# Performance work log

Hardware: AMD Instinct MI355X
Metric: run time of the kernel (lower is better)

Reference implementation:

```python
import jax, jax.numpy as jnp
import numpy as np

K = 128           # top-k
NUM_SAMPLES = 500 # perturbation samples
SIGMA = 0.05      # noise scale (forward arg sigma in the torch module)


def setup_inputs() -> dict:
    key = jax.random.key(0)
    k1, k2 = jax.random.split(key)
    x = jax.random.normal(k1, (32, 2048), dtype=jnp.float32)
    noise = jax.random.normal(k2, (32, NUM_SAMPLES, 2048), dtype=jnp.float32)
    return {"x": x, "noise": noise}


def reference(x, noise):
    # x: (b, d) scores; noise: (b, n, d) standard-normal perturbations.
    b, d = x.shape
    n = noise.shape[1]
    perturbed = x[:, None, :] + noise * SIGMA          # (b, n, d)
    _, idx = jax.lax.top_k(perturbed, K)               # (b, n, K) indices into d
    idx = jnp.sort(idx, axis=-1)                       # sorted, matching torch.sort
    # indicators[b,j,d] = mean_n one_hot(idx[b,n,j], d)
    # Computed with a scatter-add instead of materializing the (b,n,K,d) one-hot.
    bi = jnp.arange(b)[:, None, None]                  # (b,1,1)
    ki = jnp.arange(K)[None, None, :]                  # (1,1,K)
    counts = jnp.zeros((b, K, d), dtype=x.dtype).at[bi, ki, idx].add(1.0)
    indicators = counts / n                            # (b, K, d)
    return indicators, idx
```

## Files before the change

### kernel.cpp

```cpp
#include <hip/hip_runtime.h>


constexpr int B_     = 32;
constexpr int D_     = 2048;
constexpr int NS_    = 500;
constexpr int TOPK_  = 128;
constexpr int SLACK_ = 32;
constexpr float SIGMA_  = 0.05f;
constexpr int PER_LANE_ = D_ / 64;
constexpr int HALF_  = D_ / 2;
constexpr int HPL_   = HALF_ / 64;
constexpr int CAP_   = 256;
constexpr int JCHUNK_ = 8;
constexpr int CUTBIT_END_ = 14;

__device__ __forceinline__ uint32_t order_key(float f) {
  uint32_t u = __float_as_uint(f);
  return (u & 0x80000000u) ? ~u : (u | 0x80000000u);
}
__device__ __forceinline__ float inv_key(uint32_t k) {
  uint32_t u = (k & 0x80000000u) ? (k & 0x7FFFFFFFu) : ~k;
  return __uint_as_float(u);
}

__global__ __launch_bounds__(64) void ptk_cutoff(const float* __restrict__ x,
                                                 float* __restrict__ cutf,
                                                 int* __restrict__ fb_cnt) {
  if (blockIdx.x == 0 && threadIdx.x == 0) fb_cnt[0] = 0;
  const int lane = threadIdx.x & 63;
  const int b = blockIdx.x;
  const float* __restrict__ xr = x + (size_t)b * D_;
  uint32_t keys[PER_LANE_];
#pragma unroll
  for (int j = 0; j < PER_LANE_; j += 4) {
    const float4 xv = *reinterpret_cast<const float4*>(xr + lane * PER_LANE_ + j);
    keys[j + 0] = order_key(xv.x); keys[j + 1] = order_key(xv.y);
    keys[j + 2] = order_key(xv.z); keys[j + 3] = order_key(xv.w);
  }
  uint32_t prefix = 0; int k = TOPK_ + SLACK_;
#pragma unroll 1
  for (int bit = 31; bit >= CUTBIT_END_; --bit) {
    const uint32_t want = (prefix >> bit) | 1u;
    int c = 0;
#pragma unroll
    for (int j = 0; j < PER_LANE_; ++j) c += ((keys[j] >> bit) == want) ? 1 : 0;
#pragma unroll
    for (int off = 32; off >= 1; off >>= 1) c += __shfl_xor(c, off);
    if (c >= k) prefix |= (1u << bit); else k -= c;
  }
  if (lane == 0) cutf[b] = inv_key(prefix);
}

template <int NSLOT>
__device__ __forceinline__ void finish_row(const uint2* __restrict__ comp,
                                           const int C0, const int C,
                                           float* __restrict__ idx_row,
                                           const int lane, const uint64_t below) {
  uint32_t kk[NSLOT], ki[NSLOT];
#pragma unroll
  for (int s = 0; s < NSLOT; ++s) {
    const int q = (s << 6) + lane;
    const int a = (q < C0) ? q : (CAP_ + q - C0);
    const uint2 v = (q < C) ? comp[a] : make_uint2(0u, 0u);
    kk[s] = v.x; ki[s] = v.y;
  }

  uint32_t orv = 0u, andv = 0xFFFFFFFFu;
#pragma unroll
  for (int s = 0; s < NSLOT; ++s) {
    const bool valid = ((s << 6) + lane) < C;
    orv  |= valid ? kk[s] : 0u;
    andv &= valid ? kk[s] : 0xFFFFFFFFu;
  }
#pragma unroll
  for (int off = 32; off >= 1; off >>= 1) {
    orv  |= __shfl_xor(orv, off);
    andv &= __shfl_xor(andv, off);
  }
  const uint32_t diff = orv ^ andv;

  uint32_t prefix; int r;
  if (diff == 0u) {
    prefix = orv; r = TOPK_;
  } else {
    const int startbit = 31 - __clz(diff);
    prefix = (startbit == 31) ? 0u : (andv & (0xFFFFFFFFu << (startbit + 1)));
    int k = TOPK_;
    int A = C;
#pragma unroll 1
    for (int bit = startbit; bit >= 0; --bit) {
      const uint32_t want = (prefix >> bit) | 1u;
      int c = 0;
#pragma unroll
      for (int s = 0; s < NSLOT; ++s)
        c += __popcll(__ballot((kk[s] >> bit) == want));
      if (c >= k) { prefix |= (1u << bit); A = c; }
      else        { k -= c; A -= c; }
      if (A == 1) {
        uint32_t mykey = 0u; bool have = false;
#pragma unroll
        for (int s = 0; s < NSLOT; ++s) {
          const bool valid = ((s << 6) + lane) < C;
          const bool hit = valid && ((kk[s] >> bit) == (prefix >> bit));
          mykey = hit ? kk[s] : mykey;
          have |= hit;
        }
        const uint64_t mb = __ballot(have);
        const int src = __ffsll((unsigned long long)mb) - 1;
        prefix = __shfl(mykey, src);
        k = 1;
        break;
      }
    }
    r = k;
  }

  int sel_run = 0, eq_run = 0;
#pragma unroll
  for (int s = 0; s < NSLOT; ++s) {
    const bool gt = kk[s] > prefix;
    const bool eq = kk[s] == prefix;
    const uint64_t meq = __ballot(eq);
    const int eqrank = eq_run + __popcll(meq & below);
    const bool sel = gt || (eq && (eqrank < r));
    const uint64_t msel = __ballot(sel);
    if (sel) {
      const int pos = sel_run + __popcll(msel & below);
      idx_row[pos] = (float)(int)ki[s];
    }
    sel_run += __popcll(msel);
    eq_run  += __popcll(meq);
  }
}

__global__ __launch_bounds__(256, 8) void ptk_select(
    const float* __restrict__ x, const float* __restrict__ noise,
    const float* __restrict__ cutf, float* __restrict__ out_idx,
    int* __restrict__ fb_cnt, int* __restrict__ fb_list) {
  __shared__ uint2 comp[2][2 * CAP_];
  __shared__ int cnts[2][2];

  const int lane = threadIdx.x & 63;
  const int wave = threadIdx.x >> 6;
  const int pair = wave >> 1;
  const int half = wave & 1;
  const int row  = blockIdx.x * 2 + pair;
  const int b = row / NS_;

  const float* __restrict__ xr = x + (size_t)b * D_ + half * HALF_;
  const float* __restrict__ nr = noise + (size_t)row * D_ + half * HALF_;
  const int base_l = lane * HPL_;
  const int base_i = half * HALF_ + base_l;

  float p[HPL_];
#pragma unroll
  for (int j = 0; j < HPL_; j += 4) {
    const float4 nv = *reinterpret_cast<const float4*>(nr + base_l + j);
    const float4 xv = *reinterpret_cast<const float4*>(xr + base_l + j);
    p[j + 0] = fmaf(SIGMA_, nv.x, xv.x);
    p[j + 1] = fmaf(SIGMA_, nv.y, xv.y);
    p[j + 2] = fmaf(SIGMA_, nv.z, xv.z);
    p[j + 3] = fmaf(SIGMA_, nv.w, xv.w);
  }

  const float cf = cutf[b];

  uint32_t m = 0;
#pragma unroll
  for (int j = 0; j < HPL_; ++j) m |= (p[j] >= cf) ? (1u << j) : 0u;
  const int cnt = __popc(m);

  const uint64_t below = (lane == 0) ? 0ull : ((~0ull) >> (64 - lane));
  int offset = 0, Cw = 0;
#pragma unroll
  for (int t = 0; t < 5; ++t) {
    const uint64_t mb = __ballot((cnt >> t) & 1);
    offset += (int)__popcll(mb & below) << t;
    Cw     += (int)__popcll(mb) << t;
  }
  if (lane == 0) cnts[pair][half] = Cw;

  {
    int q = half * CAP_ + offset;
#pragma unroll
    for (int j = 0; j < HPL_; ++j) {
      if (m & (1u << j)) {
        comp[pair][q] = make_uint2(order_key(p[j]), (uint32_t)(base_i + j));
        ++q;
      }
    }
  }
  __syncthreads();

  if (half) return;

  const int C0 = cnts[pair][0];
  const int C1 = cnts[pair][1];
  const int C  = C0 + C1;

  float* __restrict__ idx_row = out_idx + (size_t)row * TOPK_;

  if (C >= TOPK_ && C <= CAP_) {
    const uint2* cp = comp[pair];
    if (C <= 128)       finish_row<2>(cp, C0, C, idx_row, lane, below);
    else if (C <= 192)  finish_row<3>(cp, C0, C, idx_row, lane, below);
    else                finish_row<4>(cp, C0, C, idx_row, lane, below);
  } else {
    if (lane == 0) {
      const int p_ = atomicAdd(fb_cnt, 1);
      fb_list[p_] = row;
    }
  }
}

__global__ __launch_bounds__(64) void ptk_fb(
    const float* __restrict__ x, const float* __restrict__ noise,
    const int* __restrict__ fb_cnt, const int* __restrict__ fb_list,
    float* __restrict__ out_idx) {
  const int lane = threadIdx.x & 63;
  const int cnt = fb_cnt[0];
  for (int i = blockIdx.x; i < cnt; i += (int)gridDim.x) {
    const int row = fb_list[i];
    const int b = row / NS_;
    const float* __restrict__ xr = x + (size_t)b * D_;
    const float* __restrict__ nr = noise + (size_t)row * D_;
    float* __restrict__ idx_row = out_idx + (size_t)row * TOPK_;

    const int bi = lane * PER_LANE_;
    uint32_t keys[PER_LANE_];
#pragma unroll
    for (int j = 0; j < PER_LANE_; ++j)
      keys[j] = order_key(fmaf(SIGMA_, nr[bi + j], xr[bi + j]));

    uint32_t prefix = 0; int k = TOPK_;
#pragma unroll 1
    for (int bit = 31; bit >= 0; --bit) {
      const uint32_t want = (prefix >> bit) | 1u;
      int c = 0;
#pragma unroll
      for (int j = 0; j < PER_LANE_; ++j) c += ((keys[j] >> bit) == want) ? 1 : 0;
#pragma unroll
      for (int off = 32; off >= 1; off >>= 1) c += __shfl_xor(c, off);
      if (c >= k) prefix |= (1u << bit); else k -= c;
    }
    const int r = k;

    int gt = 0, eq = 0;
#pragma unroll
    for (int j = 0; j < PER_LANE_; ++j) {
      gt += (keys[j] > prefix) ? 1 : 0;
      eq += (keys[j] == prefix) ? 1 : 0;
    }
    uint32_t incl2 = (uint32_t)gt | ((uint32_t)eq << 16);
#pragma unroll
    for (int off = 1; off < 64; off <<= 1) {
      uint32_t y = __shfl_up(incl2, (unsigned)off);
      if (lane >= off) incl2 += y;
    }
    const int gt_base = (int)(incl2 & 0xFFFFu) - gt;
    const int eq_base = (int)(incl2 >> 16) - eq;
    int pos = gt_base + min(eq_base, r);
    int eq_seen = eq_base;
#pragma unroll
    for (int j = 0; j < PER_LANE_; ++j) {
      const uint32_t kj = keys[j];
      bool s = false;
      if (kj > prefix) s = true;
      else if (kj == prefix) { s = (eq_seen < r); eq_seen++; }
      if (s) { idx_row[pos] = (float)(bi + j); pos++; }
    }
  }
}

__global__ __launch_bounds__(256) void ptk_hist(
    const float* __restrict__ out_idx, float* __restrict__ indicators) {
  __shared__ int hist[JCHUNK_][D_];

  const int tid   = threadIdx.x;
  const int b     = blockIdx.x >> 4;
  const int chunk = blockIdx.x & 15;
  const int j0    = chunk * JCHUNK_;

  int4* h4 = (int4*)hist;
  for (int t = tid; t < JCHUNK_ * D_ / 4; t += 256)
    h4[t] = make_int4(0, 0, 0, 0);
  __syncthreads();

  const float* __restrict__ src = out_idx + (size_t)b * NS_ * TOPK_ + j0;
  for (int t = tid; t < NS_ * 2; t += 256) {
    const int n = t >> 1;
    const int q = (t & 1) << 2;
    const float4 v = *reinterpret_cast<const float4*>(src + (size_t)n * TOPK_ + q);
    atomicAdd(&hist[q + 0][(int)v.x], 1);
    atomicAdd(&hist[q + 1][(int)v.y], 1);
    atomicAdd(&hist[q + 2][(int)v.z], 1);
    atomicAdd(&hist[q + 3][(int)v.w], 1);
  }
  __syncthreads();

  float4* __restrict__ dst =
      (float4*)(indicators + ((size_t)b * TOPK_ + j0) * D_);
  for (int t = tid; t < JCHUNK_ * D_ / 4; t += 256) {
    const int4 h = h4[t];
    float4 o;
    o.x = (float)h.x / (float)NS_;
    o.y = (float)h.y / (float)NS_;
    o.z = (float)h.z / (float)NS_;
    o.w = (float)h.w / (float)NS_;
    dst[t] = o;
  }
}

extern "C" void kernel_launch(void* const* d_in, const int* in_sizes, int n_in,
                              void* d_out, int out_size, void* d_ws, size_t ws_size,
                              hipStream_t stream) {
  const float* x     = (const float*)d_in[0];
  const float* noise = (const float*)d_in[1];
  float* indicators  = (float*)d_out;
  float* out_idx     = (float*)d_out + (size_t)B_ * TOPK_ * D_;
  float* cutf        = (float*)d_ws;
  int*   fb_cnt      = (int*)d_ws + 64;
  int*   fb_list     = (int*)d_ws + 128;

  hipLaunchKernelGGL(ptk_cutoff, dim3(B_), dim3(64), 0, stream, x, cutf, fb_cnt);

  const int rows = B_ * NS_;
  hipLaunchKernelGGL(ptk_select, dim3(rows / 2), dim3(256), 0, stream,
                     x, noise, cutf, out_idx, fb_cnt, fb_list);

  hipLaunchKernelGGL(ptk_fb, dim3(64), dim3(64), 0, stream,
                     x, noise, fb_cnt, fb_list, out_idx);

  hipLaunchKernelGGL(ptk_hist, dim3(B_ * 16), dim3(256), 0, stream,
                     out_idx, indicators);
}
```

Baseline: 224.3 us.

## Fold fallback exact top-k into select kernel and drop separate fallback launch

After: 220.5 us. Within noise of the previous version (-1.7%).

```diff
diff --git a/kernel.cpp b/kernel.cpp
--- a/kernel.cpp
+++ b/kernel.cpp
@@ -24,9 +24,7 @@
 }
 
 __global__ __launch_bounds__(64) void ptk_cutoff(const float* __restrict__ x,
-                                                 float* __restrict__ cutf,
-                                                 int* __restrict__ fb_cnt) {
-  if (blockIdx.x == 0 && threadIdx.x == 0) fb_cnt[0] = 0;
+                                                 float* __restrict__ cutf) {
   const int lane = threadIdx.x & 63;
   const int b = blockIdx.x;
   const float* __restrict__ xr = x + (size_t)b * D_;
@@ -135,9 +133,8 @@
 
 __global__ __launch_bounds__(256, 8) void ptk_select(
     const float* __restrict__ x, const float* __restrict__ noise,
-    const float* __restrict__ cutf, float* __restrict__ out_idx,
-    int* __restrict__ fb_cnt, int* __restrict__ fb_list) {
-  __shared__ uint2 comp[2][2 * CAP_];
+    const float* __restrict__ cutf, float* __restrict__ out_idx) {
+  __shared__ uint32_t smem[2][2048];
   __shared__ int cnts[2][2];
 
   const int lane = threadIdx.x & 63;
@@ -180,95 +177,83 @@
   }
   if (lane == 0) cnts[pair][half] = Cw;
 
+  uint2* __restrict__ comp = reinterpret_cast<uint2*>(&smem[pair][0]);
+
   {
     int q = half * CAP_ + offset;
 #pragma unroll
     for (int j = 0; j < HPL_; ++j) {
       if (m & (1u << j)) {
-        comp[pair][q] = make_uint2(order_key(p[j]), (uint32_t)(base_i + j));
+        comp[q] = make_uint2(order_key(p[j]), (uint32_t)(base_i + j));
         ++q;
       }
     }
   }
   __syncthreads();
-
-  if (half) return;
 
   const int C0 = cnts[pair][0];
   const int C1 = cnts[pair][1];
   const int C  = C0 + C1;
+  const int Ca = cnts[0][0] + cnts[0][1];
+  const int Cb = cnts[1][0] + cnts[1][1];
+  const bool anyBad = (Ca < TOPK_) || (Ca > CAP_) || (Cb < TOPK_) || (Cb > CAP_);
 
   float* __restrict__ idx_row = out_idx + (size_t)row * TOPK_;
 
-  if (C >= TOPK_ && C <= CAP_) {
-    const uint2* cp = comp[pair];
-    if (C <= 128)       finish_row<2>(cp, C0, C, idx_row, lane, below);
-    else if (C <= 192)  finish_row<3>(cp, C0, C, idx_row, lane, below);
-    else                finish_row<4>(cp, C0, C, idx_row, lane, below);
-  } else {
-    if (lane == 0) {
-      const int p_ = atomicAdd(fb_cnt, 1);
-      fb_list[p_] = row;
-    }
-  }
-}
-
-__global__ __launch_bounds__(64) void ptk_fb(
-    const float* __restrict__ x, const float* __restrict__ noise,
-    const int* __restrict__ fb_cnt, const int* __restrict__ fb_list,
-    float* __restrict__ out_idx) {
-  const int lane = threadIdx.x & 63;
-  const int cnt = fb_cnt[0];
-  for (int i = blockIdx.x; i < cnt; i += (int)gridDim.x) {
-    const int row = fb_list[i];
-    const int b = row / NS_;
-    const float* __restrict__ xr = x + (size_t)b * D_;
-    const float* __restrict__ nr = noise + (size_t)row * D_;
-    float* __restrict__ idx_row = out_idx + (size_t)row * TOPK_;
-
-    const int bi = lane * PER_LANE_;
-    uint32_t keys[PER_LANE_];
-#pragma unroll
-    for (int j = 0; j < PER_LANE_; ++j)
-      keys[j] = order_key(fmaf(SIGMA_, nr[bi + j], xr[bi + j]));
-
+  if (!anyBad) {
+    if (half) return;
+    if (C <= 128)       finish_row<2>(comp, C0, C, idx_row, lane, below);
+    else if (C <= 192)  finish_row<3>(comp, C0, C, idx_row, lane, below);
+    else                finish_row<4>(comp, C0, C, idx_row, lane, below);
+    return;
+  }
+
+  const bool myBad = (C < TOPK_) || (C > CAP_);
+  if (myBad) {
+    uint32_t* __restrict__ dst = &smem[pair][half * HALF_ + base_l];
+#pragma unroll
+    for (int j = 0; j < HPL_; j += 4) {
+      uint4 v;
+      v.x = order_key(p[j + 0]); v.y = order_key(p[j + 1]);
+      v.z = order_key(p[j + 2]); v.w = order_key(p[j + 3]);
+      *reinterpret_cast<uint4*>(dst + j) = v;
+    }
+  }
+  __syncthreads();
+
+  if (half) return;
+  if (myBad) {
+    const uint32_t* __restrict__ keys = &smem[pair][0];
     uint32_t prefix = 0; int k = TOPK_;
 #pragma unroll 1
     for (int bit = 31; bit >= 0; --bit) {
       const uint32_t want = (prefix >> bit) | 1u;
       int c = 0;
-#pragma unroll
-      for (int j = 0; j < PER_LANE_; ++j) c += ((keys[j] >> bit) == want) ? 1 : 0;
-#pragma unroll
-      for (int off = 32; off >= 1; off >>= 1) c += __shfl_xor(c, off);
+#pragma unroll 1
+      for (int t = 0; t < D_; t += 64)
+        c += (int)__popcll(__ballot((keys[t + lane] >> bit) == want));
       if (c >= k) prefix |= (1u << bit); else k -= c;
     }
     const int r = k;
 
-    int gt = 0, eq = 0;
-#pragma unroll
-    for (int j = 0; j < PER_LANE_; ++j) {
-      gt += (keys[j] > prefix) ? 1 : 0;
-      eq += (keys[j] == prefix) ? 1 : 0;
-    }
-    uint32_t incl2 = (uint32_t)gt | ((uint32_t)eq << 16);
-#pragma unroll
-    for (int off = 1; off < 64; off <<= 1) {
-      uint32_t y = __shfl_up(incl2, (unsigned)off);
-      if (lane >= off) incl2 += y;
-    }
-    const int gt_base = (int)(incl2 & 0xFFFFu) - gt;
-    const int eq_base = (int)(incl2 >> 16) - eq;
-    int pos = gt_base + min(eq_base, r);
-    int eq_seen = eq_base;
-#pragma unroll
-    for (int j = 0; j < PER_LANE_; ++j) {
-      const uint32_t kj = keys[j];
-      bool s = false;
-      if (kj > prefix) s = true;
-      else if (kj == prefix) { s = (eq_seen < r); eq_seen++; }
-      if (s) { idx_row[pos] = (float)(bi + j); pos++; }
-    }
+    int sel_run = 0, eq_run = 0;
+#pragma unroll 1
+    for (int t = 0; t < D_; t += 64) {
+      const uint32_t kj = keys[t + lane];
+      const bool gt = kj > prefix;
+      const bool eq = kj == prefix;
+      const uint64_t meq = __ballot(eq);
+      const int eqrank = eq_run + __popcll(meq & below);
+      const bool sel = gt || (eq && (eqrank < r));
+      const uint64_t msel = __ballot(sel);
+      if (sel) idx_row[sel_run + __popcll(msel & below)] = (float)(t + lane);
+      sel_run += __popcll(msel);
+      eq_run  += __popcll(meq);
+    }
+  } else {
+    if (C <= 128)       finish_row<2>(comp, C0, C, idx_row, lane, below);
+    else if (C <= 192)  finish_row<3>(comp, C0, C, idx_row, lane, below);
+    else                finish_row<4>(comp, C0, C, idx_row, lane, below);
   }
 }
 
@@ -319,17 +304,12 @@
   float* indicators  = (float*)d_out;
   float* out_idx     = (float*)d_out + (size_t)B_ * TOPK_ * D_;
   float* cutf        = (float*)d_ws;
-  int*   fb_cnt      = (int*)d_ws + 64;
-  int*   fb_list     = (int*)d_ws + 128;
-
-  hipLaunchKernelGGL(ptk_cutoff, dim3(B_), dim3(64), 0, stream, x, cutf, fb_cnt);
+
+  hipLaunchKernelGGL(ptk_cutoff, dim3(B_), dim3(64), 0, stream, x, cutf);
 
   const int rows = B_ * NS_;
   hipLaunchKernelGGL(ptk_select, dim3(rows / 2), dim3(256), 0, stream,
-                     x, noise, cutf, out_idx, fb_cnt, fb_list);
-
-  hipLaunchKernelGGL(ptk_fb, dim3(64), dim3(64), 0, stream,
-                     x, noise, fb_cnt, fb_list, out_idx);
+                     x, noise, cutf, out_idx);
 
   hipLaunchKernelGGL(ptk_hist, dim3(B_ * 16), dim3(256), 0, stream,
                      out_idx, indicators);
```
